# Kernel tuning notes

Hardware: AMD Instinct MI355X
Metric: run time of the kernel (lower is better)

The kernel has to match this reference:

```python
import jax, jax.numpy as jnp
import numpy as np


def setup_inputs() -> dict:
    key = jax.random.key(0)
    kQ, kS, kR, kP = jax.random.split(key, 4)
    B, C, Cv = 4, 128, 128
    h, w = 128, 128
    H, W = 256, 256
    k = 16
    Q = jax.random.normal(kQ, (B, C, h, w), dtype=jnp.float32)
    S = jax.random.normal(kS, (B, C, H, W), dtype=jnp.float32)
    R = jax.random.normal(kR, (B, Cv, H, W), dtype=jnp.float32)
    Pos = jax.random.randint(kP, (B, 2, h, w, k), 0, 256, dtype=jnp.int32)
    return {"Q": Q, "S": S, "R": R, "Pos": Pos}


def reference(Q, S, R, Pos):
    # Q: (B, C, h, w); S: (B, C, H, W); R: (B, Cv, H, W); Pos: (B, 2, h, w, k)
    B, C, h, w = Q.shape
    _, Cv, H, W = R.shape
    k = Pos.shape[-1]
    hw = h * w

    # Flatten (x, y) neighbor coords into linear indices over H*W: (B, hw*k)
    flat_idx = (Pos[:, 0].reshape(B, -1).astype(jnp.int32) * W
                + Pos[:, 1].reshape(B, -1).astype(jnp.int32))

    # Gather epipolar neighborhoods (vectorized over batch, no python loop)
    KeyG = jnp.take_along_axis(S.reshape(B, C, H * W), flat_idx[:, None, :], axis=2)
    ValG = jnp.take_along_axis(R.reshape(B, Cv, H * W), flat_idx[:, None, :], axis=2)
    Key = KeyG.reshape(B, C, hw, k)    # (B, C, hw, k)
    Val = ValG.reshape(B, Cv, hw, k)   # (B, Cv, hw, k)

    Qr = Q.transpose(0, 2, 3, 1).reshape(B, hw, C)          # (B, hw, C)
    score = jnp.einsum('bpc,bcpk->bpk', Qr, Key)            # (B, hw, k)
    attn = jax.nn.softmax(score, axis=-1)                   # (B, hw, k)
    out = jnp.einsum('bpk,bcpk->bpc', attn, Val)            # (B, hw, Cv)

    buffer = out.reshape(B, h, w, Cv).transpose(0, 3, 1, 2)  # (B, Cv, h, w)
    M_right_to_left = attn[:, :, None, :]                    # (B, hw, 1, k) as in torch
    return buffer, M_right_to_left
```

## Files before the change

### kernel.cpp

```cpp
#include <hip/hip_runtime.h>

constexpr int B  = 4;
constexpr int C  = 128;
constexpr int hw = 16384;
constexpr int W_ = 256;
constexpr int HW = 65536;
constexpr int K  = 16;
constexpr int P_TILE = 16;
constexpr int BLOCKS_PER_BATCH = hw / P_TILE;

typedef __attribute__((ext_vector_type(8))) _Float16 half8;

__global__ __launch_bounds__(256) void transpose_kv_f16(
    const float* __restrict__ S, const float* __restrict__ R,
    _Float16* __restrict__ KV)
{
    __shared__ float tile[64][65];
    const int z   = blockIdx.z;
    const int n0  = blockIdx.x * 64;
    const int c0  = blockIdx.y * 64;
    const int tid = threadIdx.x;
    _Float16* dbase = KV + (size_t)z * HW * 256;

    const float* srcs[2] = { S + (size_t)z * C * HW, R + (size_t)z * C * HW };

    #pragma unroll
    for (int t = 0; t < 2; ++t) {
        const float* s = srcs[t];
        #pragma unroll
        for (int i = 0; i < 4; ++i) {
            const int cl = (tid >> 4) + i * 16;
            const int x0 = (tid & 15) * 4;
            const float4 v = *reinterpret_cast<const float4*>(
                &s[(size_t)(c0 + cl) * HW + n0 + x0]);
            tile[cl][x0]     = v.x;
            tile[cl][x0 + 1] = v.y;
            tile[cl][x0 + 2] = v.z;
            tile[cl][x0 + 3] = v.w;
        }
        __syncthreads();
        #pragma unroll
        for (int it = 0; it < 2; ++it) {
            const int nl = (tid >> 3) + it * 32;
            const int u  = tid & 7;
            half8 hv;
            #pragma unroll
            for (int i = 0; i < 8; ++i)
                hv[i] = (_Float16)tile[8 * u + i][nl];
            *reinterpret_cast<half8*>(
                dbase + (size_t)(n0 + nl) * 256 + t * 128 + c0 + 8 * u) = hv;
        }
        __syncthreads();
    }
}

__global__ __launch_bounds__(256) void attn_gather_kv(
    const float* __restrict__ Q, const int* __restrict__ Pos,
    const _Float16* __restrict__ KV,
    float* __restrict__ outBuf, float* __restrict__ outM, int b0)
{
    __shared__ float q_s[P_TILE][132];
    __shared__ float out_s[P_TILE][132];

    const int tid = threadIdx.x;
    const int bb  = blockIdx.x / BLOCKS_PER_BATCH;
    const int b   = b0 + bb;
    const int p0  = (blockIdx.x % BLOCKS_PER_BATCH) * P_TILE;

    for (int i = tid; i < P_TILE * C; i += 256) {
        int c = i >> 4, pl0 = i & 15;
        q_s[pl0][c] = Q[((size_t)(b * C + c)) * hw + p0 + pl0];
    }
    const int pl = tid >> 4;
    const int cg = tid & 15;
    const int p  = p0 + pl;
    int myidx;
    {
        const int rr = Pos[(((size_t)(b * 2 + 0) * hw) + p) * K + cg];
        const int cc = Pos[(((size_t)(b * 2 + 1) * hw) + p) * K + cg];
        myidx = rr * W_ + cc;
    }
    __syncthreads();

    float qf[8];
    #pragma unroll
    for (int i = 0; i < 8; ++i) qf[i] = q_s[pl][cg * 8 + i];

    float m = -1e30f, l = 0.f, myscore = 0.f;
    float acc[8];
    #pragma unroll
    for (int i = 0; i < 8; ++i) acc[i] = 0.f;

    const half8* base = reinterpret_cast<const half8*>(KV) + (size_t)bb * HW * 32;

    #pragma unroll
    for (int kc = 0; kc < K; kc += 8) {
        half8 kreg[8], vreg[8];
        #pragma unroll
        for (int r = 0; r < 8; ++r) {
            const int ridx = __shfl(myidx, kc + r, 16);
            const half8* row = base + (size_t)ridx * 32;
            kreg[r] = row[cg];
            vreg[r] = row[16 + cg];
        }
        #pragma unroll
        for (int r = 0; r < 8; ++r) {
            float part = 0.f;
            #pragma unroll
            for (int i = 0; i < 8; ++i) part += qf[i] * (float)kreg[r][i];
            #pragma unroll
            for (int off = 1; off < 16; off <<= 1) part += __shfl_xor(part, off);
            const float mn    = fmaxf(m, part);
            const float scale = __expf(m - mn);
            const float e     = __expf(part - mn);
            l = l * scale + e;
            #pragma unroll
            for (int i = 0; i < 8; ++i) acc[i] = acc[i] * scale + e * (float)vreg[r][i];
            m = mn;
            if (cg == kc + r) myscore = part;
        }
    }

    const float inv_l = 1.0f / l;
    const float attn  = __expf(myscore - m) * inv_l;
    outM[((size_t)b * hw + p) * K + cg] = attn;
    #pragma unroll
    for (int i = 0; i < 8; ++i) out_s[pl][cg * 8 + i] = acc[i] * inv_l;
    __syncthreads();
    for (int i = tid; i < P_TILE * C; i += 256) {
        int c = i >> 4, pl3 = i & 15;
        outBuf[((size_t)(b * C + c)) * hw + p0 + pl3] = out_s[pl3][c];
    }
}

__global__ __launch_bounds__(256) void attn_direct(
    const float* __restrict__ Q, const float* __restrict__ S, const float* __restrict__ R,
    const int* __restrict__ Pos, float* __restrict__ outBuf, float* __restrict__ outM)
{
    __shared__ float q_s[P_TILE][132];
    __shared__ float attn_s[P_TILE][17];
    __shared__ int   idx_s[P_TILE][K];
    __shared__ float out_s[P_TILE][132];

    const int tid = threadIdx.x;
    const int b   = blockIdx.x / BLOCKS_PER_BATCH;
    const int p0  = (blockIdx.x % BLOCKS_PER_BATCH) * P_TILE;

    for (int i = tid; i < P_TILE * C; i += 256) {
        int c = i >> 4, pl0 = i & 15;
        q_s[pl0][c] = Q[((size_t)(b * C + c)) * hw + p0 + pl0];
    }
    const int pl = tid >> 4;
    const int kk = tid & 15;
    const int p  = p0 + pl;
    const int rr = Pos[(((size_t)(b * 2 + 0) * hw) + p) * K + kk];
    const int cc = Pos[(((size_t)(b * 2 + 1) * hw) + p) * K + kk];
    const int idx = rr * W_ + cc;
    idx_s[pl][kk] = idx;
    __syncthreads();

    float score = 0.f;
    {
        const float* srow = S + (size_t)b * C * HW + idx;
        for (int c = 0; c < C; ++c) score += q_s[pl][c] * srow[(size_t)c * HW];
    }
    float mx = score;
    #pragma unroll
    for (int off = 1; off < 16; off <<= 1) mx = fmaxf(mx, __shfl_xor(mx, off));
    float e = __expf(score - mx);
    float ssum = e;
    #pragma unroll
    for (int off = 1; off < 16; off <<= 1) ssum += __shfl_xor(ssum, off);
    const float attn = e / ssum;
    outM[((size_t)b * hw + p) * K + kk] = attn;
    attn_s[pl][kk] = attn;
    __syncthreads();

    {
        const int pl2 = tid >> 4;
        const int cg  = tid & 15;
        float acc[8];
        #pragma unroll
        for (int i = 0; i < 8; ++i) acc[i] = 0.f;
        for (int k2 = 0; k2 < K; ++k2) {
            const float a = attn_s[pl2][k2];
            const float* rw = R + (size_t)b * C * HW + idx_s[pl2][k2];
            #pragma unroll
            for (int i = 0; i < 8; ++i) acc[i] += a * rw[(size_t)(cg * 8 + i) * HW];
        }
        #pragma unroll
        for (int i = 0; i < 8; ++i) out_s[pl2][cg * 8 + i] = acc[i];
    }
    __syncthreads();
    for (int i = tid; i < P_TILE * C; i += 256) {
        int c = i >> 4, pl3 = i & 15;
        outBuf[((size_t)(b * C + c)) * hw + p0 + pl3] = out_s[pl3][c];
    }
}

extern "C" void kernel_launch(void* const* d_in, const int* in_sizes, int n_in,
                              void* d_out, int out_size, void* d_ws, size_t ws_size,
                              hipStream_t stream)
{
    (void)in_sizes; (void)n_in; (void)out_size;
    const float* Q  = (const float*)d_in[0];
    const float* S  = (const float*)d_in[1];
    const float* R  = (const float*)d_in[2];
    const int*  Pos = (const int*)d_in[3];
    float* outBuf = (float*)d_out;
    float* outM   = outBuf + (size_t)B * C * hw;

    const size_t fullBytes     = (size_t)B * HW * 256 * sizeof(_Float16);
    const size_t perBatchBytes = (size_t)HW * 256 * sizeof(_Float16);

    dim3 tb(256);
    if (ws_size >= fullBytes) {
        _Float16* KVt = (_Float16*)d_ws;
        dim3 tg(HW / 64, C / 64, B);
        transpose_kv_f16<<<tg, tb, 0, stream>>>(S, R, KVt);
        attn_gather_kv<<<dim3(B * BLOCKS_PER_BATCH), 256, 0, stream>>>(
            Q, Pos, KVt, outBuf, outM, 0);
    } else if (ws_size >= perBatchBytes) {
        _Float16* KVt = (_Float16*)d_ws;
        dim3 tg(HW / 64, C / 64, 1);
        for (int b = 0; b < B; ++b) {
            transpose_kv_f16<<<tg, tb, 0, stream>>>(
                S + (size_t)b * C * HW, R + (size_t)b * C * HW, KVt);
            attn_gather_kv<<<dim3(BLOCKS_PER_BATCH), 256, 0, stream>>>(
                Q, Pos, KVt, outBuf, outM, b);
        }
    } else {
        attn_direct<<<dim3(B * BLOCKS_PER_BATCH), 256, 0, stream>>>(
            Q, S, R, Pos, outBuf, outM);
    }
}
```

Before: 403.0 us.

## Restructure KV transpose to stage fp16 tile of 128 positions with XOR swizzle

The transpose kernel now has each block handle 128 spatial positions across all 256 channels (S and R together). It converts to fp16 before writing to shared memory and uses an XOR-swizzled layout to avoid bank conflicts. Each thread then writes a full 16-byte row chunk, so global writes cover whole 512-byte rows per position. The aim is lower LDS traffic and better-coalesced stores for the transpose pass. The cost is 64KB of LDS per block, which lowers occupancy, and fewer, larger blocks.

```diff
diff --git a/kernel.cpp b/kernel.cpp
--- a/kernel.cpp
+++ b/kernel.cpp
@@ -9,48 +9,59 @@
 constexpr int P_TILE = 16;
 constexpr int BLOCKS_PER_BATCH = hw / P_TILE;
 
+typedef __attribute__((ext_vector_type(4))) _Float16 half4v;
 typedef __attribute__((ext_vector_type(8))) _Float16 half8;
 
 __global__ __launch_bounds__(256) void transpose_kv_f16(
     const float* __restrict__ S, const float* __restrict__ R,
     _Float16* __restrict__ KV)
 {
-    __shared__ float tile[64][65];
+    __shared__ _Float16 kv[256 * 128];
     const int z   = blockIdx.z;
-    const int n0  = blockIdx.x * 64;
-    const int c0  = blockIdx.y * 64;
+    const int n0  = blockIdx.x * 128;
     const int tid = threadIdx.x;
+    const int n4  = tid & 31;
+    const int rg  = tid >> 5;
+
+    const float* s = S + (size_t)z * C * HW;
+    const float* r = R + (size_t)z * C * HW;
+
+    #pragma unroll
+    for (int i = 0; i < 16; ++i) {
+        const int cl = rg + 8 * i;
+        const float4 vs = *reinterpret_cast<const float4*>(
+            &s[(size_t)cl * HW + n0 + 4 * n4]);
+        const float4 vr = *reinterpret_cast<const float4*>(
+            &r[(size_t)cl * HW + n0 + 4 * n4]);
+        const int chS = cl;
+        const int chR = cl + 128;
+        const int npS = n4 ^ ((chS >> 3) & 31);
+        const int npR = n4 ^ ((chR >> 3) & 31);
+        half4v hs, hr;
+        hs[0] = (_Float16)vs.x; hs[1] = (_Float16)vs.y;
+        hs[2] = (_Float16)vs.z; hs[3] = (_Float16)vs.w;
+        hr[0] = (_Float16)vr.x; hr[1] = (_Float16)vr.y;
+        hr[2] = (_Float16)vr.z; hr[3] = (_Float16)vr.w;
+        *reinterpret_cast<half4v*>(&kv[chS * 128 + 4 * npS]) = hs;
+        *reinterpret_cast<half4v*>(&kv[chR * 128 + 4 * npR]) = hr;
+    }
+    __syncthreads();
+
     _Float16* dbase = KV + (size_t)z * HW * 256;
-
-    const float* srcs[2] = { S + (size_t)z * C * HW, R + (size_t)z * C * HW };
-
-    #pragma unroll
-    for (int t = 0; t < 2; ++t) {
-        const float* s = srcs[t];
-        #pragma unroll
-        for (int i = 0; i < 4; ++i) {
-            const int cl = (tid >> 4) + i * 16;
-            const int x0 = (tid & 15) * 4;
-            const float4 v = *reinterpret_cast<const float4*>(
-                &s[(size_t)(c0 + cl) * HW + n0 + x0]);
-            tile[cl][x0]     = v.x;
-            tile[cl][x0 + 1] = v.y;
-            tile[cl][x0 + 2] = v.z;
-            tile[cl][x0 + 3] = v.w;
-        }
-        __syncthreads();
-        #pragma unroll
-        for (int it = 0; it < 2; ++it) {
-            const int nl = (tid >> 3) + it * 32;
-            const int u  = tid & 7;
-            half8 hv;
-            #pragma unroll
-            for (int i = 0; i < 8; ++i)
-                hv[i] = (_Float16)tile[8 * u + i][nl];
-            *reinterpret_cast<half8*>(
-                dbase + (size_t)(n0 + nl) * 256 + t * 128 + c0 + 8 * u) = hv;
-        }
-        __syncthreads();
+    const int u  = tid & 31;
+    const int rl = tid >> 5;
+    #pragma unroll
+    for (int p = 0; p < 16; ++p) {
+        const int nn = rl + 8 * p;
+        const int q  = nn >> 2;
+        const int rm = nn & 3;
+        half8 hv;
+        #pragma unroll
+        for (int i = 0; i < 8; ++i) {
+            const int ch = 8 * u + i;
+            hv[i] = kv[ch * 128 + ((q ^ u) << 2) + rm];
+        }
+        *reinterpret_cast<half8*>(&dbase[(size_t)(n0 + nn) * 256 + 8 * u]) = hv;
     }
 }
 
@@ -216,13 +227,13 @@
     dim3 tb(256);
     if (ws_size >= fullBytes) {
         _Float16* KVt = (_Float16*)d_ws;
-        dim3 tg(HW / 64, C / 64, B);
+        dim3 tg(HW / 128, 1, B);
         transpose_kv_f16<<<tg, tb, 0, stream>>>(S, R, KVt);
         attn_gather_kv<<<dim3(B * BLOCKS_PER_BATCH), 256, 0, stream>>>(
             Q, Pos, KVt, outBuf, outM, 0);
     } else if (ws_size >= perBatchBytes) {
         _Float16* KVt = (_Float16*)d_ws;
-        dim3 tg(HW / 64, C / 64, 1);
+        dim3 tg(HW / 128, 1, 1);
         for (int b = 0; b < B; ++b) {
             transpose_kv_f16<<<tg, tb, 0, stream>>>(
                 S + (size_t)b * C * HW, R + (size_t)b * C * HW, KVt);
```

Result: no change. 397.4 us (-1.4%).

## Pipeline KV transpose with double-buffered async global-to-LDS loads

Applied to the files above, without the earlier changes.

Rewrites the fp32-to-fp16 S/R transpose kernel. Each block now loops over 16 chunks of 64 positions covering all 256 key and value channels. It prefetches the next chunk straight into LDS with global_load_lds (16-byte loads and an XOR swizzle) while converting the current chunk. The goal is to hide global read latency and remove register staging. The cost is 128KB of LDS per block, which limits each CU to one block and lowers occupancy.

```diff
diff --git a/kernel.cpp b/kernel.cpp
--- a/kernel.cpp
+++ b/kernel.cpp
@@ -9,49 +9,83 @@
 constexpr int P_TILE = 16;
 constexpr int BLOCKS_PER_BATCH = hw / P_TILE;
 
+constexpr int CHUNK_N = 64;
+constexpr int CPB     = 16;
+constexpr int CHUNKS_PER_BATCH_T = HW / CHUNK_N;
+
 typedef __attribute__((ext_vector_type(8))) _Float16 half8;
+
+__device__ __forceinline__ void async_copy16(const float* gsrc, float* ldst)
+{
+    __builtin_amdgcn_global_load_lds(
+        (const __attribute__((address_space(1))) void*)gsrc,
+        (__attribute__((address_space(3))) void*)ldst,
+        16, 0, 0);
+}
 
 __global__ __launch_bounds__(256) void transpose_kv_f16(
     const float* __restrict__ S, const float* __restrict__ R,
     _Float16* __restrict__ KV)
 {
-    __shared__ float tile[64][65];
-    const int z   = blockIdx.z;
-    const int n0  = blockIdx.x * 64;
-    const int c0  = blockIdx.y * 64;
-    const int tid = threadIdx.x;
-    _Float16* dbase = KV + (size_t)z * HW * 256;
-
-    const float* srcs[2] = { S + (size_t)z * C * HW, R + (size_t)z * C * HW };
-
-    #pragma unroll
-    for (int t = 0; t < 2; ++t) {
-        const float* s = srcs[t];
-        #pragma unroll
-        for (int i = 0; i < 4; ++i) {
-            const int cl = (tid >> 4) + i * 16;
-            const int x0 = (tid & 15) * 4;
-            const float4 v = *reinterpret_cast<const float4*>(
-                &s[(size_t)(c0 + cl) * HW + n0 + x0]);
-            tile[cl][x0]     = v.x;
-            tile[cl][x0 + 1] = v.y;
-            tile[cl][x0 + 2] = v.z;
-            tile[cl][x0 + 3] = v.w;
-        }
-        __syncthreads();
-        #pragma unroll
-        for (int it = 0; it < 2; ++it) {
-            const int nl = (tid >> 3) + it * 32;
-            const int u  = tid & 7;
+    __shared__ float bufs[2][256 * CHUNK_N];
+    const int tid  = threadIdx.x;
+    const int lane = tid & 63;
+    const int w64  = tid >> 6;
+    const int u    = tid & 31;
+    const int rl   = tid >> 5;
+
+    auto STAGE = [&](float* buf, int g) {
+        const int z  = g >> 10;
+        const int n0 = (g & 1023) << 6;
+        const float* sB = S + (size_t)z * C * HW;
+        const float* rB = R + (size_t)z * C * HW;
+        #pragma unroll
+        for (int j = 0; j < 16; ++j) {
+            const int r0 = w64 * 64 + j * 4;
+            const int ch = r0 + (lane >> 4);
+            const int qs = lane & 15;
+            const int q  = qs ^ ((ch >> 3) & 15);
+            const float* gp = ((ch < 128) ? sB + (size_t)ch * HW
+                                          : rB + (size_t)(ch - 128) * HW)
+                              + n0 + 4 * q;
+            async_copy16(gp, buf + r0 * CHUNK_N);
+        }
+    };
+
+    auto DRAIN = [&](const float* buf, int g) {
+        const int z  = g >> 10;
+        const int n0 = (g & 1023) << 6;
+        _Float16* dbase = KV + (size_t)z * HW * 256;
+        #pragma unroll
+        for (int p = 0; p < 8; ++p) {
+            const int n  = rl + 8 * p;
+            const int nq = n >> 2;
+            const int rm = n & 3;
             half8 hv;
             #pragma unroll
-            for (int i = 0; i < 8; ++i)
-                hv[i] = (_Float16)tile[8 * u + i][nl];
+            for (int i = 0; i < 8; ++i) {
+                const int ch = 8 * u + i;
+                const int qs = nq ^ ((ch >> 3) & 15);
+                hv[i] = (_Float16)buf[ch * CHUNK_N + qs * 4 + rm];
+            }
             *reinterpret_cast<half8*>(
-                dbase + (size_t)(n0 + nl) * 256 + t * 128 + c0 + 8 * u) = hv;
-        }
-        __syncthreads();
-    }
+                &dbase[(size_t)(n0 + n) * 256 + 8 * u]) = hv;
+        }
+    };
+
+    const int g0 = blockIdx.x * CPB;
+
+    STAGE(bufs[0], g0);
+    for (int t = 0; t < CPB - 1; ++t) {
+        STAGE(bufs[(t + 1) & 1], g0 + t + 1);
+        asm volatile("s_waitcnt vmcnt(16)" ::: "memory");
+        __builtin_amdgcn_s_barrier();
+        DRAIN(bufs[t & 1], g0 + t);
+        __builtin_amdgcn_s_barrier();
+    }
+    asm volatile("s_waitcnt vmcnt(0)" ::: "memory");
+    __builtin_amdgcn_s_barrier();
+    DRAIN(bufs[(CPB - 1) & 1], g0 + CPB - 1);
 }
 
 __global__ __launch_bounds__(256) void attn_gather_kv(
@@ -216,15 +250,14 @@
     dim3 tb(256);
     if (ws_size >= fullBytes) {
         _Float16* KVt = (_Float16*)d_ws;
-        dim3 tg(HW / 64, C / 64, B);
-        transpose_kv_f16<<<tg, tb, 0, stream>>>(S, R, KVt);
+        transpose_kv_f16<<<dim3(B * CHUNKS_PER_BATCH_T / CPB), tb, 0, stream>>>(
+            S, R, KVt);
         attn_gather_kv<<<dim3(B * BLOCKS_PER_BATCH), 256, 0, stream>>>(
             Q, Pos, KVt, outBuf, outM, 0);
     } else if (ws_size >= perBatchBytes) {
         _Float16* KVt = (_Float16*)d_ws;
-        dim3 tg(HW / 64, C / 64, 1);
         for (int b = 0; b < B; ++b) {
-            transpose_kv_f16<<<tg, tb, 0, stream>>>(
+            transpose_kv_f16<<<dim3(CHUNKS_PER_BATCH_T / CPB), tb, 0, stream>>>(
                 S + (size_t)b * C * HW, R + (size_t)b * C * HW, KVt);
             attn_gather_kv<<<dim3(BLOCKS_PER_BATCH), 256, 0, stream>>>(
                 Q, Pos, KVt, outBuf, outM, b);
```

Measured after the change: 401.2 us. No clear change (-0.4%).
